# Kernel optimization log

Hardware: AMD Instinct MI355X
Metric: run time of the kernel (lower is better)

The kernel has to match this reference:

```python
import jax, jax.numpy as jnp
import numpy as np

NUM_HEADS = 16
N_EMBD = 1024
HEAD_SIZE = N_EMBD // NUM_HEADS
BLOCK_SIZE = 2048
B, T = 4, 2048


def setup_inputs() -> dict:
    key = jax.random.key(0)
    ks = jax.random.split(key, 6)
    x = jax.random.normal(ks[0], (B, T, N_EMBD), dtype=jnp.float32)
    s = 1.0 / np.sqrt(N_EMBD)
    # per-head q/k/v projections (bias=False), stacked over heads: [H, D, hs]
    Wq = jax.random.uniform(ks[1], (NUM_HEADS, N_EMBD, HEAD_SIZE), minval=-s, maxval=s, dtype=jnp.float32)
    Wk = jax.random.uniform(ks[2], (NUM_HEADS, N_EMBD, HEAD_SIZE), minval=-s, maxval=s, dtype=jnp.float32)
    Wv = jax.random.uniform(ks[3], (NUM_HEADS, N_EMBD, HEAD_SIZE), minval=-s, maxval=s, dtype=jnp.float32)
    # output projection nn.Linear(n_embd, n_embd): weight [D, D] (out, in) + bias [D]
    Wo = jax.random.uniform(ks[4], (N_EMBD, N_EMBD), minval=-s, maxval=s, dtype=jnp.float32)
    bo = jax.random.uniform(ks[5], (N_EMBD,), minval=-s, maxval=s, dtype=jnp.float32)
    return {"x": x, "Wq": Wq, "Wk": Wk, "Wv": Wv, "Wo": Wo, "bo": bo}


def _mha(x, Wq, Wk, Wv, Wo, bo):
    # project all heads at once: [B,T,D] x [H,D,hs] -> [B,H,T,hs]
    q = jnp.einsum("btd,hds->bhts", x, Wq)
    k = jnp.einsum("btd,hds->bhts", x, Wk)
    v = jnp.einsum("btd,hds->bhts", x, Wv)
    scale = jnp.asarray(HEAD_SIZE, x.dtype) ** -0.5
    scores = jnp.einsum("bhqs,bhks->bhqk", q, k) * scale  # [B,H,T,T]
    T_ = x.shape[1]
    causal = jnp.tril(jnp.ones((T_, T_), dtype=bool))
    scores = jnp.where(causal[None, None], scores, jnp.asarray(-jnp.inf, x.dtype))
    att = jax.nn.softmax(scores, axis=-1)
    out = jnp.einsum("bhqk,bhks->bhqs", att, v)  # [B,H,T,hs]
    # concat heads along last dim: [B,T,H*hs]
    out = out.transpose(0, 2, 1, 3).reshape(x.shape[0], T_, N_EMBD)
    # output projection (dropout=0.0 -> identity)
    return out @ Wo.T + bo


def reference(x, Wq, Wk, Wv, Wo, bo):
    return _mha(x, Wq, Wk, Wv, Wo, bo)
```

## Files before the change

kernel.cpp:

```cpp
#include <hip/hip_runtime.h>
#include <hip/hip_bf16.h>
#include <stdint.h>

typedef __bf16 bf16;
typedef __attribute__((ext_vector_type(8))) __bf16 bf16x8;
typedef __attribute__((ext_vector_type(4))) float f32x4;

#define NH     16
#define DM     1024
#define HS     64
#define BATCH  4
#define SEQ    2048
#define N_XE   (BATCH * SEQ * DM)
#define N_WOE  (DM * DM)
#define NKT    16

__device__ __forceinline__ void async16(void* lds, const void* g) {
  __builtin_amdgcn_global_load_lds(
      (const uint32_t __attribute__((address_space(1)))*)g,
      (uint32_t __attribute__((address_space(3)))*)lds,
      16, 0, 0);
}

__device__ __forceinline__ f32x4 mfma16(bf16x8 a, bf16x8 b, f32x4 c) {
  return __builtin_amdgcn_mfma_f32_16x16x32_bf16(a, b, c, 0, 0, 0);
}

__global__ void detect_mode(const unsigned short* __restrict__ x, int* flag) {
  int lane = threadIdx.x & 63;
  unsigned short v = x[2 * lane];
  int e = (v >> 7) & 0xFF;
  int sane = (e >= 90 && e <= 160) ? 1 : 0;
  #pragma unroll
  for (int s = 1; s < 64; s <<= 1) sane += __shfl_xor(sane, s, 64);
  if (threadIdx.x == 0) *flag = (sane >= 48) ? 0 : 1;
}

__global__ __launch_bounds__(256)
void convert_in(const void* __restrict__ x, const void* __restrict__ Wo,
                bf16* __restrict__ xb, bf16* __restrict__ Wob,
                const int* __restrict__ flagp) {
  const int f32m = *flagp;
  size_t base = ((size_t)blockIdx.x * 256 + threadIdx.x) * 8;
  const void* src; bf16* dst; size_t off;
  if (base < (size_t)N_XE) { src = x;  dst = xb;  off = base; }
  else                     { src = Wo; dst = Wob; off = base - N_XE; }
  if (f32m) {
    const float* s = (const float*)src + off;
    float4 a = *(const float4*)s;
    float4 b = *(const float4*)(s + 4);
    bf16x8 o;
    o[0] = (bf16)a.x; o[1] = (bf16)a.y; o[2] = (bf16)a.z; o[3] = (bf16)a.w;
    o[4] = (bf16)b.x; o[5] = (bf16)b.y; o[6] = (bf16)b.z; o[7] = (bf16)b.w;
    *(bf16x8*)(dst + off) = o;
  } else {
    *(bf16x8*)(dst + off) = *(const bf16x8*)((const bf16*)src + off);
  }
}

__global__ __launch_bounds__(256)
void transpose_w(const void* __restrict__ Wq, const void* __restrict__ Wk,
                 const void* __restrict__ Wv, bf16* __restrict__ WT,
                 const int* __restrict__ flagp) {
  __shared__ bf16 Ts[64][72];
  const int f32m = *flagp;
  const void* W = (blockIdx.y == 0) ? Wq : (blockIdx.y == 1) ? Wk : Wv;
  bf16* dst = WT + (size_t)blockIdx.y * DM * DM;
  const int h  = blockIdx.x >> 4;
  const int d0 = (blockIdx.x & 15) * 64;
  const int tid = threadIdx.x;
  #pragma unroll
  for (int p = 0; p < 2; ++p) {
    int idx = p * 256 + tid;
    int dr = idx >> 3, c = idx & 7;
    size_t eoff = (size_t)(h * DM + d0 + dr) * HS + c * 8;
    bf16x8 v;
    if (f32m) {
      const float* s = (const float*)W + eoff;
      #pragma unroll
      for (int j = 0; j < 8; ++j) v[j] = (bf16)s[j];
    } else {
      v = *(const bf16x8*)((const bf16*)W + eoff);
    }
    #pragma unroll
    for (int j = 0; j < 8; ++j) Ts[c * 8 + j][dr] = v[j];
  }
  __syncthreads();
  #pragma unroll
  for (int p = 0; p < 2; ++p) {
    int idx = p * 256 + tid;
    int sr = idx >> 3, c = idx & 7;
    bf16x8 v = *(const bf16x8*)(&Ts[sr][c * 8]);
    *(bf16x8*)(dst + (size_t)(h * 64 + sr) * DM + d0 + c * 8) = v;
  }
}

__device__ __forceinline__ bf16x8 ldsfrag(const bf16* base, int r, int kk, int fg) {
  return *(const bf16x8*)(base + r * 64 + (((kk * 4 + fg) ^ (r & 7)) * 8));
}

template<typename EpiF>
__device__ __forceinline__ void gemm256_8ph(const bf16* __restrict__ A,
                                            const bf16* __restrict__ BT,
                                            int m0, int n0, EpiF epi) {
  __shared__ bf16 As[2][256 * 64];
  __shared__ bf16 Bs[2][256 * 64];
  const int tid  = threadIdx.x;
  const int wid  = tid >> 6, lane = tid & 63;
  const int wr = wid >> 2, wc = wid & 3;
  const int fr = lane & 15, fg = lane >> 4;
  const int srow = tid >> 3;
  const int scg  = (tid & 7) ^ (srow & 7);
  f32x4 acc[8][4] = {};

  auto STAGE_PART = [&](int buf, int kt, int j) {
    async16((char*)&As[buf][0] + j * 8192 + wid * 1024,
            A + (size_t)(m0 + j * 64 + srow) * DM + kt * 64 + scg * 8);
    async16((char*)&Bs[buf][0] + j * 8192 + wid * 1024,
            BT + (size_t)(n0 + j * 64 + srow) * DM + kt * 64 + scg * 8);
  };

  #pragma unroll
  for (int j = 0; j < 4; ++j) STAGE_PART(0, 0, j);

  bf16x8 af[8], bfr[8];
  #pragma unroll 1
  for (int kt = 0; kt < NKT; ++kt) {
    const int buf = kt & 1;
    const bool pre = (kt + 1) < NKT;
    #pragma unroll
    for (int q = 0; q < 4; ++q) {
      if (q == 0) {
        if (pre) {
          STAGE_PART(buf ^ 1, kt + 1, 0);
          asm volatile("s_waitcnt vmcnt(2)" ::: "memory");
        } else {
          asm volatile("s_waitcnt vmcnt(0)" ::: "memory");
        }
        __builtin_amdgcn_s_barrier();
        asm volatile("" ::: "memory");
        #pragma unroll
        for (int i = 0; i < 4; ++i) {
          int r = wr * 128 + i * 16 + fr;
          #pragma unroll
          for (int kk = 0; kk < 2; ++kk)
            af[i * 2 + kk] = ldsfrag(&As[buf][0], r, kk, fg);
        }
        #pragma unroll
        for (int i = 0; i < 4; ++i) {
          int r = wc * 64 + i * 16 + fr;
          #pragma unroll
          for (int kk = 0; kk < 2; ++kk)
            bfr[i * 2 + kk] = ldsfrag(&Bs[buf][0], r, kk, fg);
        }
      } else {
        if (q == 2) {
          #pragma unroll
          for (int i = 0; i < 4; ++i) {
            int r = wr * 128 + 64 + i * 16 + fr;
            #pragma unroll
            for (int kk = 0; kk < 2; ++kk)
              af[i * 2 + kk] = ldsfrag(&As[buf][0], r, kk, fg);
          }
        }
        if (pre) STAGE_PART(buf ^ 1, kt + 1, q);
        __builtin_amdgcn_s_barrier();
        asm volatile("" ::: "memory");
      }
      const int mio = (q >> 1) * 4, nio = (q & 1) * 2;
      __builtin_amdgcn_s_setprio(1);
      #pragma unroll
      for (int i = 0; i < 4; ++i)
        #pragma unroll
        for (int nj = 0; nj < 2; ++nj)
          #pragma unroll
          for (int kk = 0; kk < 2; ++kk)
            acc[mio + i][nio + nj] =
                mfma16(af[i * 2 + kk], bfr[(nio + nj) * 2 + kk], acc[mio + i][nio + nj]);
      __builtin_amdgcn_s_setprio(0);
      __builtin_amdgcn_s_barrier();
      asm volatile("" ::: "memory");
    }
  }
  #pragma unroll
  for (int mi = 0; mi < 8; ++mi)
    #pragma unroll
    for (int ni = 0; ni < 4; ++ni)
      #pragma unroll
      for (int rr = 0; rr < 4; ++rr) {
        int m = m0 + wr * 128 + mi * 16 + fg * 4 + rr;
        int n = wc * 64 + ni * 16 + fr;
        epi(m, n, acc[mi][ni][rr]);
      }
}

__global__ __launch_bounds__(512, 2)
void qkv_gemm(const bf16* __restrict__ x, const bf16* __restrict__ WT,
              bf16* __restrict__ Qb, bf16* __restrict__ Kb, bf16* __restrict__ Vt) {
  const int xcd = blockIdx.x & 7;
  const int k   = blockIdx.x >> 3;
  const int m_tile = xcd * 4 + k / 12;
  const int nz = k % 12;
  const int z  = nz >> 2;
  const int n_tile = nz & 3;
  const int m0 = m_tile * 256;
  const int nb = n_tile * 256;
  const bf16* BT = WT + (size_t)z * DM * DM + (size_t)nb * DM;
  gemm256_8ph(x, BT, m0, 0, [&](int m, int nrel, float v) {
    int n = nb + nrel;
    int b = m >> 11, t = m & 2047, h = n >> 6, s = n & 63;
    if (z == 0)
      Qb[((size_t)(b * NH + h) * SEQ + t) * HS + s] = (bf16)v;
    else if (z == 1)
      Kb[((size_t)(b * NH + h) * SEQ + t) * HS + s] = (bf16)v;
    else
      Vt[((size_t)(b * NH + h) * HS + s) * SEQ + t] = (bf16)v;
  });
}

__global__ __launch_bounds__(512, 2)
void out_gemm(const bf16* __restrict__ att, const bf16* __restrict__ Wob,
              const void* __restrict__ bo, void* __restrict__ out,
              const int* __restrict__ flagp) {
  const int f32m = *flagp;
  const int xcd = blockIdx.x & 7;
  const int k   = blockIdx.x >> 3;
  const int m_tile = xcd * 4 + (k >> 2);
  const int n_tile = k & 3;
  const int m0 = m_tile * 256;
  const int nb = n_tile * 256;
  const bf16* BT = Wob + (size_t)nb * DM;
  gemm256_8ph(att, BT, m0, 0, [&](int m, int nrel, float v) {
    int n = nb + nrel;
    float bv = f32m ? ((const float*)bo)[n] : (float)((const bf16*)bo)[n];
    float o = v + bv;
    if (f32m) ((float*)out)[(size_t)m * DM + n] = o;
    else      ((bf16*)out)[(size_t)m * DM + n] = (bf16)o;
  });
}

#define KVB  64
__global__ __launch_bounds__(256, 2)
void attn_kernel(const bf16* __restrict__ Qb, const bf16* __restrict__ Kb,
                 const bf16* __restrict__ Vt, bf16* __restrict__ att) {
  __shared__ bf16 Ks[2][64][64];
  __shared__ bf16 Vs[2][64][64];
  __shared__ bf16 Ps[4][2][16][64];
  const int wave = threadIdx.x >> 6, lane = threadIdx.x & 63;
  const int fr = lane & 15, fg = lane >> 4;
  const int pair = blockIdx.x;
  const int bh = blockIdx.y;
  const bf16* Qp = Qb + (size_t)bh * SEQ * HS;
  const bf16* Kp = Kb + (size_t)bh * SEQ * HS;
  const bf16* Vp = Vt + (size_t)bh * HS * SEQ;
  const int b = bh >> 4, h = bh & 15;

  const int srow8 = lane >> 3;
  const int schk  = (lane & 7) ^ srow8;

  #pragma unroll
  for (int seg = 0; seg < 2; ++seg) {
    const int qb = seg == 0 ? (15 - pair) : pair;
    const int q0 = qb * 128 + wave * 32;
    const int kv_hi = q0 + 32;
    const int nt = (qb + 1) * 2;

    bf16x8 qf[2][2];
    #pragma unroll
    for (int qt = 0; qt < 2; ++qt)
      #pragma unroll
      for (int hh = 0; hh < 2; ++hh)
        qf[qt][hh] = *(const bf16x8*)(Qp + (size_t)(q0 + qt * 16 + fr) * HS + hh * 32 + fg * 8);

    float rs[2][4] = {};
    f32x4 accO[2][4] = {};

    auto STAGE = [&](int buf, int kvb) {
      #pragma unroll
      for (int i = 0; i < 2; ++i) {
        int r8 = wave * 16 + i * 8;
        async16(&Ks[buf][r8][0], Kp + (size_t)(kvb + r8 + srow8) * HS + schk * 8);
        async16(&Vs[buf][r8][0], Vp + (size_t)(r8 + srow8) * SEQ + kvb + schk * 8);
      }
    };

    STAGE(0, 0);
    for (int t = 0; t < nt; ++t) {
      const int buf = t & 1;
      const int kvb = t * KVB;
      if (t + 1 < nt) {
        STAGE(buf ^ 1, kvb + KVB);
        asm volatile("s_waitcnt vmcnt(4)" ::: "memory");
      } else {
        asm volatile("s_waitcnt vmcnt(0)" ::: "memory");
      }
      __builtin_amdgcn_s_barrier();
      if (kvb < kv_hi) {
        bf16x8 kf[4][2];
        #pragma unroll
        for (int s = 0; s < 4; ++s)
          #pragma unroll
          for (int hh = 0; hh < 2; ++hh)
            kf[s][hh] = *(const bf16x8*)(&Ks[buf][s * 16 + fr][((hh * 4 + fg) ^ (fr & 7)) * 8]);
        asm volatile("s_waitcnt lgkmcnt(0)" ::: "memory");

        #pragma unroll
        for (int qt = 0; qt < 2; ++qt) {
          f32x4 sc[4];
          #pragma unroll
          for (int s = 0; s < 4; ++s) {
            sc[s] = f32x4{0.f, 0.f, 0.f, 0.f};
            sc[s] = mfma16(qf[qt][0], kf[s][0], sc[s]);
            sc[s] = mfma16(qf[qt][1], kf[s][1], sc[s]);
          }
          #pragma unroll
          for (int s = 0; s < 4; ++s)
            #pragma unroll
            for (int r = 0; r < 4; ++r) {
              int qrow = q0 + qt * 16 + fg * 4 + r;
              int col  = kvb + s * 16 + fr;
              float p = __expf(sc[s][r] * 0.125f);
              p = (col <= qrow) ? p : 0.f;
              rs[qt][r] += p;
              int row = fg * 4 + r;
              int swz = (s * 2 + (fr >> 3)) ^ (row & 7);
              Ps[wave][qt][row][swz * 8 + (fr & 7)] = (bf16)p;
            }
        }
        asm volatile("s_waitcnt lgkmcnt(0)" ::: "memory");
        __builtin_amdgcn_sched_barrier(0);
        bf16x8 pf[2][2];
        #pragma unroll
        for (int qt = 0; qt < 2; ++qt)
          #pragma unroll
          for (int kc = 0; kc < 2; ++kc)
            pf[qt][kc] = *(const bf16x8*)(&Ps[wave][qt][fr][(((kc * 4 + fg) ^ (fr & 7))) * 8]);
        #pragma unroll
        for (int st = 0; st < 4; ++st) {
          bf16x8 vf0 = *(const bf16x8*)(&Vs[buf][st * 16 + fr][((fg) ^ (fr & 7)) * 8]);
          bf16x8 vf1 = *(const bf16x8*)(&Vs[buf][st * 16 + fr][((4 + fg) ^ (fr & 7)) * 8]);
          #pragma unroll
          for (int qt = 0; qt < 2; ++qt) {
            accO[qt][st] = mfma16(pf[qt][0], vf0, accO[qt][st]);
            accO[qt][st] = mfma16(pf[qt][1], vf1, accO[qt][st]);
          }
        }
      }
      __builtin_amdgcn_s_barrier();
    }

    #pragma unroll
    for (int sh = 1; sh < 16; sh <<= 1)
      #pragma unroll
      for (int qt = 0; qt < 2; ++qt)
        #pragma unroll
        for (int r = 0; r < 4; ++r)
          rs[qt][r] += __shfl_xor(rs[qt][r], sh, 64);
    #pragma unroll
    for (int qt = 0; qt < 2; ++qt)
      #pragma unroll
      for (int st = 0; st < 4; ++st)
        #pragma unroll
        for (int r = 0; r < 4; ++r) {
          int qrow = q0 + qt * 16 + fg * 4 + r;
          float o = accO[qt][st][r] / rs[qt][r];
          att[((size_t)(b * SEQ + qrow)) * DM + h * 64 + st * 16 + fr] = (bf16)o;
        }
  }
}

extern "C" void kernel_launch(void* const* d_in, const int* in_sizes, int n_in,
                              void* d_out, int out_size, void* d_ws, size_t ws_size,
                              hipStream_t stream) {
  const void* x  = d_in[0];
  const void* Wq = d_in[1];
  const void* Wk = d_in[2];
  const void* Wv = d_in[3];
  const void* Wo = d_in[4];
  const void* bo = d_in[5];

  char* ws = (char*)d_ws;
  int*  flag = (int*)ws;
  bf16* xb  = (bf16*)(ws + 256);
  bf16* WT  = (bf16*)(ws + 256 + ((size_t)16 << 20));
  bf16* Wob = (bf16*)(ws + 256 + ((size_t)22 << 20));
  bf16* Qb  = (bf16*)(ws + 256 + ((size_t)24 << 20));
  bf16* Kb  = (bf16*)(ws + 256 + ((size_t)40 << 20));
  bf16* Vt  = (bf16*)(ws + 256 + ((size_t)56 << 20));
  bf16* att = xb;

  detect_mode<<<1, 64, 0, stream>>>((const unsigned short*)x, flag);
  convert_in<<<(N_XE + N_WOE) / 2048, 256, 0, stream>>>(x, Wo, xb, Wob, flag);
  transpose_w<<<dim3(256, 3), 256, 0, stream>>>(Wq, Wk, Wv, WT, flag);
  qkv_gemm<<<dim3(384), 512, 0, stream>>>(xb, WT, Qb, Kb, Vt);
  attn_kernel<<<dim3(8, BATCH * NH), 256, 0, stream>>>(Qb, Kb, Vt, att);
  out_gemm<<<dim3(128), 512, 0, stream>>>(att, Wob, bo, d_out, flag);
}
```

Baseline: 320.8 us.

## Replace 8-phase double-buffered GEMM with triple-buffered BK=32 pipeline

Rewrites the shared 256x256 GEMM mainloop used by the QKV and output projections. The K tile shrinks from 64 to 32, buffering goes from two stages to three with two tiles prefetched, and the four-phase interleaved schedule with many barriers becomes one load-then-compute phase per k-step with a new LDS swizzle. The aim is to cut barrier count and hide global latency with deeper prefetch. The cost is twice as many k iterations, a different LDS bank-conflict pattern, and less overlap of LDS reads with MFMA issue inside each step.

```diff
diff --git a/kernel.cpp b/kernel.cpp
--- a/kernel.cpp
+++ b/kernel.cpp
@@ -13,7 +13,6 @@
 #define SEQ    2048
 #define N_XE   (BATCH * SEQ * DM)
 #define N_WOE  (DM * DM)
-#define NKT    16
 
 __device__ __forceinline__ void async16(void* lds, const void* g) {
   __builtin_amdgcn_global_load_lds(
@@ -95,92 +94,68 @@
   }
 }
 
-__device__ __forceinline__ bf16x8 ldsfrag(const bf16* base, int r, int kk, int fg) {
-  return *(const bf16x8*)(base + r * 64 + (((kk * 4 + fg) ^ (r & 7)) * 8));
-}
-
+#define GKT 32
 template<typename EpiF>
-__device__ __forceinline__ void gemm256_8ph(const bf16* __restrict__ A,
-                                            const bf16* __restrict__ BT,
-                                            int m0, int n0, EpiF epi) {
-  __shared__ bf16 As[2][256 * 64];
-  __shared__ bf16 Bs[2][256 * 64];
+__device__ __forceinline__ void gemm256_bt(const bf16* __restrict__ A,
+                                           const bf16* __restrict__ BT,
+                                           int m0, int n0, EpiF epi) {
+  __shared__ bf16 As[3][256 * 32];
+  __shared__ bf16 Bs[3][256 * 32];
   const int tid  = threadIdx.x;
   const int wid  = tid >> 6, lane = tid & 63;
   const int wr = wid >> 2, wc = wid & 3;
   const int fr = lane & 15, fg = lane >> 4;
-  const int srow = tid >> 3;
-  const int scg  = (tid & 7) ^ (srow & 7);
+  const int srow = lane >> 2;
+  const int schk = (lane & 3) ^ ((lane >> 3) & 3);
   f32x4 acc[8][4] = {};
 
-  auto STAGE_PART = [&](int buf, int kt, int j) {
-    async16((char*)&As[buf][0] + j * 8192 + wid * 1024,
-            A + (size_t)(m0 + j * 64 + srow) * DM + kt * 64 + scg * 8);
-    async16((char*)&Bs[buf][0] + j * 8192 + wid * 1024,
-            BT + (size_t)(n0 + j * 64 + srow) * DM + kt * 64 + scg * 8);
+  auto STAGE = [&](int kt, int buf) {
+    #pragma unroll
+    for (int i = 0; i < 2; ++i) {
+      int row = wid * 32 + i * 16 + srow;
+      async16((char*)&As[buf][0] + wid * 2048 + i * 1024,
+              A + (size_t)(m0 + row) * DM + kt * 32 + schk * 8);
+      async16((char*)&Bs[buf][0] + wid * 2048 + i * 1024,
+              BT + (size_t)(n0 + row) * DM + kt * 32 + schk * 8);
+    }
   };
 
-  #pragma unroll
-  for (int j = 0; j < 4; ++j) STAGE_PART(0, 0, j);
-
-  bf16x8 af[8], bfr[8];
+  STAGE(0, 0); STAGE(1, 1);
+  int cbuf = 0, sbuf = 2;
   #pragma unroll 1
-  for (int kt = 0; kt < NKT; ++kt) {
-    const int buf = kt & 1;
-    const bool pre = (kt + 1) < NKT;
-    #pragma unroll
-    for (int q = 0; q < 4; ++q) {
-      if (q == 0) {
-        if (pre) {
-          STAGE_PART(buf ^ 1, kt + 1, 0);
-          asm volatile("s_waitcnt vmcnt(2)" ::: "memory");
-        } else {
-          asm volatile("s_waitcnt vmcnt(0)" ::: "memory");
-        }
-        __builtin_amdgcn_s_barrier();
-        asm volatile("" ::: "memory");
-        #pragma unroll
-        for (int i = 0; i < 4; ++i) {
-          int r = wr * 128 + i * 16 + fr;
-          #pragma unroll
-          for (int kk = 0; kk < 2; ++kk)
-            af[i * 2 + kk] = ldsfrag(&As[buf][0], r, kk, fg);
-        }
-        #pragma unroll
-        for (int i = 0; i < 4; ++i) {
-          int r = wc * 64 + i * 16 + fr;
-          #pragma unroll
-          for (int kk = 0; kk < 2; ++kk)
-            bfr[i * 2 + kk] = ldsfrag(&Bs[buf][0], r, kk, fg);
-        }
-      } else {
-        if (q == 2) {
-          #pragma unroll
-          for (int i = 0; i < 4; ++i) {
-            int r = wr * 128 + 64 + i * 16 + fr;
-            #pragma unroll
-            for (int kk = 0; kk < 2; ++kk)
-              af[i * 2 + kk] = ldsfrag(&As[buf][0], r, kk, fg);
-          }
-        }
-        if (pre) STAGE_PART(buf ^ 1, kt + 1, q);
-        __builtin_amdgcn_s_barrier();
-        asm volatile("" ::: "memory");
-      }
-      const int mio = (q >> 1) * 4, nio = (q & 1) * 2;
-      __builtin_amdgcn_s_setprio(1);
-      #pragma unroll
-      for (int i = 0; i < 4; ++i)
-        #pragma unroll
-        for (int nj = 0; nj < 2; ++nj)
-          #pragma unroll
-          for (int kk = 0; kk < 2; ++kk)
-            acc[mio + i][nio + nj] =
-                mfma16(af[i * 2 + kk], bfr[(nio + nj) * 2 + kk], acc[mio + i][nio + nj]);
-      __builtin_amdgcn_s_setprio(0);
-      __builtin_amdgcn_s_barrier();
-      asm volatile("" ::: "memory");
-    }
+  for (int kt = 0; kt < GKT; ++kt) {
+    if (kt + 2 < GKT) {
+      STAGE(kt + 2, sbuf);
+      sbuf = (sbuf == 2) ? 0 : sbuf + 1;
+      asm volatile("s_waitcnt vmcnt(8)" ::: "memory");
+    } else if (kt + 1 < GKT) {
+      asm volatile("s_waitcnt vmcnt(4)" ::: "memory");
+    } else {
+      asm volatile("s_waitcnt vmcnt(0)" ::: "memory");
+    }
+    __builtin_amdgcn_s_barrier();
+    const bf16* Ab = &As[cbuf][0];
+    const bf16* Bb = &Bs[cbuf][0];
+    bf16x8 af[8], bv[4];
+    #pragma unroll
+    for (int i = 0; i < 8; ++i) {
+      int r = wr * 128 + i * 16 + fr;
+      af[i] = *(const bf16x8*)(Ab + r * 32 + ((fg ^ ((r >> 1) & 3)) * 8));
+    }
+    #pragma unroll
+    for (int i = 0; i < 4; ++i) {
+      int r = wc * 64 + i * 16 + fr;
+      bv[i] = *(const bf16x8*)(Bb + r * 32 + ((fg ^ ((r >> 1) & 3)) * 8));
+    }
+    __builtin_amdgcn_s_setprio(1);
+    #pragma unroll
+    for (int mi = 0; mi < 8; ++mi)
+      #pragma unroll
+      for (int ni = 0; ni < 4; ++ni)
+        acc[mi][ni] = mfma16(af[mi], bv[ni], acc[mi][ni]);
+    __builtin_amdgcn_s_setprio(0);
+    __builtin_amdgcn_s_barrier();
+    cbuf = (cbuf == 2) ? 0 : cbuf + 1;
   }
   #pragma unroll
   for (int mi = 0; mi < 8; ++mi)
@@ -202,11 +177,10 @@
   const int m_tile = xcd * 4 + k / 12;
   const int nz = k % 12;
   const int z  = nz >> 2;
-  const int n_tile = nz & 3;
+  const int nb = (nz & 3) * 256;
   const int m0 = m_tile * 256;
-  const int nb = n_tile * 256;
   const bf16* BT = WT + (size_t)z * DM * DM + (size_t)nb * DM;
-  gemm256_8ph(x, BT, m0, 0, [&](int m, int nrel, float v) {
+  gemm256_bt(x, BT, m0, 0, [&](int m, int nrel, float v) {
     int n = nb + nrel;
     int b = m >> 11, t = m & 2047, h = n >> 6, s = n & 63;
     if (z == 0)
@@ -226,11 +200,10 @@
   const int xcd = blockIdx.x & 7;
   const int k   = blockIdx.x >> 3;
   const int m_tile = xcd * 4 + (k >> 2);
-  const int n_tile = k & 3;
+  const int nb = (k & 3) * 256;
   const int m0 = m_tile * 256;
-  const int nb = n_tile * 256;
   const bf16* BT = Wob + (size_t)nb * DM;
-  gemm256_8ph(att, BT, m0, 0, [&](int m, int nrel, float v) {
+  gemm256_bt(att, BT, m0, 0, [&](int m, int nrel, float v) {
     int n = nb + nrel;
     float bv = f32m ? ((const float*)bo)[n] : (float)((const bf16*)bo)[n];
     float o = v + bv;
```

Result: slower. 338.6 us (+5.6%).
